# Kernel tuning notes

Hardware: AMD Instinct MI355X
Metric: run time of the kernel (lower is better)

The kernel has to match this reference:

```python
import jax, jax.numpy as jnp
import numpy as np

B, N, S, K, D = 8, 8192, 1024, 32, 64
RADIUS = 0.2
MLP = [64, 64, 128]
C_IN = 3 + D


def _fps(pts):
    # pts: [N,3] -> [S] farthest-point indices (deterministic start at index 0,
    # matching pytorch3d.sample_farthest_points default random_start_point=False)
    def body(carry, _):
        d, last = carry
        dd = jnp.sum((pts - pts[last]) ** 2, axis=-1)
        d = jnp.minimum(d, dd)
        return (d, jnp.argmax(d)), last
    init = (jnp.full((pts.shape[0],), 1e10, pts.dtype), jnp.asarray(0))
    _, idxs = jax.lax.scan(body, init, None, length=S)
    return idxs


def _ball_query(new_xyz, xyz):
    # new_xyz [B,S,3], xyz [B,N,3] -> idx [B,S,K]
    # classic PointNet++ ball query: first K points (by index order) within radius;
    # queries with fewer than K neighbors are padded by replicating the first hit.
    sqr = jnp.sum((new_xyz[:, :, None, :] - xyz[:, None, :, :]) ** 2, axis=-1)  # [B,S,N]
    cand = jnp.where(sqr <= RADIUS ** 2,
                     jnp.arange(N, dtype=jnp.int32)[None, None, :],
                     jnp.int32(N))
    idx = -jax.lax.top_k(-cand, K)[0]  # K smallest valid indices, ascending
    first = idx[..., :1]
    return jnp.where(idx == N, first, idx)


def _gather(arr, idx):
    # arr [B,N,C], idx [B,S,K] -> [B,S,K,C]
    return jax.vmap(lambda a, i: a[i])(arr, idx)


def _forward(xyz, points, attention, w0, b0, w1, b1, w2, b2):
    x = xyz.transpose(0, 2, 1)        # [B,N,3]
    p = points.transpose(0, 2, 1)     # [B,N,D]
    a = attention.transpose(0, 2, 1)  # [B,N,1]
    fps_idx = jax.vmap(_fps)(x)                      # [B,S]
    new_xyz = jax.vmap(lambda q, i: q[i])(x, fps_idx)  # [B,S,3]
    idx = _ball_query(new_xyz, x)                    # [B,S,K]
    g_norm = _gather(x, idx) - new_xyz[:, :, None, :]   # [B,S,K,3]
    feat = jnp.concatenate([g_norm, _gather(p, idx)], axis=-1)  # [B,S,K,3+D]
    new_att = jnp.mean(_gather(a, idx), axis=-2).reshape(x.shape[0], 1, -1)  # [B,1,S]
    # shared MLP (1x1 Conv2d == per-point dense), no BN (bn=False)
    h = jax.nn.relu(jnp.einsum('bskc,oc->bsko', feat, w0) + b0)
    h = jax.nn.relu(jnp.einsum('bskc,oc->bsko', h, w1) + b1)
    h = jax.nn.relu(jnp.einsum('bskc,oc->bsko', h, w2) + b2)
    new_points = jnp.max(h, axis=2)  # max-pool over nsample -> [B,S,C_out]
    return new_xyz.transpose(0, 2, 1), new_points.transpose(0, 2, 1), new_att


def setup_inputs() -> dict:
    key = jax.random.key(0)
    ks = jax.random.split(key, 9)
    xyz = jax.random.uniform(ks[0], (B, 3, N), dtype=jnp.float32)  # unit cube
    points = jax.random.normal(ks[1], (B, D, N), dtype=jnp.float32)
    attention = jax.random.uniform(ks[2], (B, 1, N), dtype=jnp.float32)
    cin = C_IN
    w0 = jax.random.normal(ks[3], (MLP[0], cin), dtype=jnp.float32) / np.sqrt(cin)
    b0 = jnp.zeros((MLP[0],), jnp.float32)
    w1 = jax.random.normal(ks[4], (MLP[1], MLP[0]), dtype=jnp.float32) / np.sqrt(MLP[0])
    b1 = jnp.zeros((MLP[1],), jnp.float32)
    w2 = jax.random.normal(ks[5], (MLP[2], MLP[1]), dtype=jnp.float32) / np.sqrt(MLP[1])
    b2 = jnp.zeros((MLP[2],), jnp.float32)
    return {"xyz": xyz, "points": points, "attention": attention,
            "w0": w0, "b0": b0, "w1": w1, "b1": b1, "w2": w2, "b2": b2}


def reference(xyz, points, attention, w0, b0, w1, b1, w2, b2):
    return _forward(xyz, points, attention, w0, b0, w1, b1, w2, b2)
```

## Files before the change

kernel.cpp:

```cpp
#include <hip/hip_runtime.h>

#define NPTS 8192
#define NSAMP 1024
#define NBATCH 8
#define KNB 32

typedef float f32x2 __attribute__((ext_vector_type(2)));
typedef unsigned long long u64;

__device__ __forceinline__ f32x2 pk_add(f32x2 a, f32x2 b) {
  f32x2 d; asm("v_pk_add_f32 %0, %1, %2" : "=v"(d) : "v"(a), "v"(b)); return d;
}
__device__ __forceinline__ f32x2 pk_mul(f32x2 a, f32x2 b) {
  f32x2 d; asm("v_pk_mul_f32 %0, %1, %2" : "=v"(d) : "v"(a), "v"(b)); return d;
}

#define DPP_FMAX_ROUND(v, CTRL)                                                        \
  do {                                                                                 \
    int _b = __float_as_int(v);                                                        \
    int _p = __builtin_amdgcn_update_dpp(_b, _b, CTRL, 0xF, 0xF, false);               \
    (v) = fmaxf((v), __int_as_float(_p));                                              \
  } while (0)

#define DPP_FMIN_ROUND(v, CTRL)                                                        \
  do {                                                                                 \
    int _b = __float_as_int(v);                                                        \
    int _p = __builtin_amdgcn_update_dpp(_b, _b, CTRL, 0xF, 0xF, false);               \
    (v) = fminf((v), __int_as_float(_p));                                              \
  } while (0)

#define DPP_UMIN_ROUND(v, CTRL)                                                        \
  do {                                                                                 \
    unsigned _p = (unsigned)__builtin_amdgcn_update_dpp((int)(v), (int)(v), CTRL,      \
                                                        0xF, 0xF, false);              \
    if (_p < (v)) (v) = _p;                                                            \
  } while (0)

#define DPP_MIN_ROUND(k, CTRL)                                                         \
  do {                                                                                 \
    unsigned _lo = (unsigned)(k), _hi = (unsigned)((k) >> 32);                         \
    unsigned _plo = (unsigned)__builtin_amdgcn_update_dpp((int)_lo, (int)_lo, CTRL,    \
                                                          0xF, 0xF, false);            \
    unsigned _phi = (unsigned)__builtin_amdgcn_update_dpp((int)_hi, (int)_hi, CTRL,    \
                                                          0xF, 0xF, false);            \
    u64 _ok = (((u64)_phi) << 32) | _plo;                                              \
    if (_ok < (k)) (k) = _ok;                                                          \
  } while (0)

__device__ __forceinline__ float sqdist_rn(float px, float py, float pz,
                                           float qx, float qy, float qz) {
  float dx = px - qx, dy = py - qy, dz = pz - qz;
  return __fadd_rn(__fadd_rn(__fmul_rn(dx, dx), __fmul_rn(dy, dy)), __fmul_rn(dz, dz));
}

__global__ __launch_bounds__(512) void fps_kernel(const float* __restrict__ xyz,
                                                  float* __restrict__ out_newxyz) {
  __shared__ __align__(16) char smem_raw[NPTS * 3 * 4];
  u64* sbuf = reinterpret_cast<u64*>(smem_raw);
  float* cds = reinterpret_cast<float*>(smem_raw);
  __shared__ u64 wkeys[2][8];

  const int b = blockIdx.x;
  const int tid = threadIdx.x;
  const int lane = tid & 63;
  const int wv = tid >> 6;
  const float* xb = xyz + (size_t)b * 3 * NPTS;

  for (int j = 0; j < 16; j++) {
    int n = tid + j * 512;
    float x = xb[n];
    sbuf[n] = (((u64)__float_as_uint(x)) << 32) | (u64)n;
  }
  __syncthreads();

  for (unsigned k = 2; k <= (unsigned)NPTS; k <<= 1) {
    for (unsigned jm = k >> 1; jm > 0; jm >>= 1) {
      for (int p = 0; p < 16; p++) {
        unsigned i = (unsigned)tid + (unsigned)p * 512u;
        unsigned ixj = i ^ jm;
        if (ixj > i) {
          u64 a = sbuf[i], c = sbuf[ixj];
          bool up = ((i & k) == 0);
          if ((a > c) == up) { sbuf[i] = c; sbuf[ixj] = a; }
        }
      }
      __syncthreads();
    }
  }

  f32x2 X2[8], Y2[8], Z2[8], D2[8];
  unsigned idxp[8];
  float txmin = 1e30f, txmax = -1e30f;
#pragma unroll
  for (int j = 0; j < 8; j++) {
    u64 k0 = sbuf[tid * 16 + 2 * j];
    u64 k1 = sbuf[tid * 16 + 2 * j + 1];
    unsigned n0 = (unsigned)k0 & 8191u, n1 = (unsigned)k1 & 8191u;
    float x0 = __uint_as_float((unsigned)(k0 >> 32));
    float x1 = __uint_as_float((unsigned)(k1 >> 32));
    X2[j].x = x0; X2[j].y = x1;
    Y2[j].x = xb[NPTS + n0];     Y2[j].y = xb[NPTS + n1];
    Z2[j].x = xb[2 * NPTS + n0]; Z2[j].y = xb[2 * NPTS + n1];
    D2[j].x = 1e10f;             D2[j].y = 1e10f;
    idxp[j] = n0 | (n1 << 16);
    txmin = fminf(txmin, fminf(x0, x1));
    txmax = fmaxf(txmax, fmaxf(x0, x1));
  }
  DPP_FMIN_ROUND(txmin, 0x111); DPP_FMIN_ROUND(txmin, 0x112);
  DPP_FMIN_ROUND(txmin, 0x114); DPP_FMIN_ROUND(txmin, 0x118);
  DPP_FMIN_ROUND(txmin, 0x142); DPP_FMIN_ROUND(txmin, 0x143);
  DPP_FMAX_ROUND(txmax, 0x111); DPP_FMAX_ROUND(txmax, 0x112);
  DPP_FMAX_ROUND(txmax, 0x114); DPP_FMAX_ROUND(txmax, 0x118);
  DPP_FMAX_ROUND(txmax, 0x142); DPP_FMAX_ROUND(txmax, 0x143);
  const float xlo = __int_as_float(__builtin_amdgcn_readlane(__float_as_int(txmin), 63));
  const float xhi = __int_as_float(__builtin_amdgcn_readlane(__float_as_int(txmax), 63));
  __syncthreads();

#pragma unroll
  for (int j = 0; j < 8; j++) {
    unsigned n0 = idxp[j] & 0xFFFFu, n1 = idxp[j] >> 16;
    cds[n0 * 3 + 0] = X2[j].x; cds[n0 * 3 + 1] = Y2[j].x; cds[n0 * 3 + 2] = Z2[j].x;
    cds[n1 * 3 + 0] = X2[j].y; cds[n1 * 3 + 1] = Y2[j].y; cds[n1 * 3 + 2] = Z2[j].y;
  }
  __syncthreads();

  float sx = cds[0], sy = cds[1], sz = cds[2];
  unsigned c0i = 0, c1i = 0;
  float bv_cache = 1e10f;
  u64 key_cache = ~0ull;

  for (int t = 0; t < NSAMP; t++) {
    float gap = fmaxf(fmaxf(xlo - sx, sx - xhi), 0.0f);
    float lb = __fmul_rn(gap, gap);

    if (lb < bv_cache) {
      f32x2 nqx, nqy, nqz;
      nqx.x = -sx; nqx.y = -sx;
      nqy.x = -sy; nqy.y = -sy;
      nqz.x = -sz; nqz.y = -sz;
      float bvx = -1.0f, bvy = -1.0f;
#pragma unroll
      for (int j = 0; j < 8; j++) {
        f32x2 dx = pk_add(X2[j], nqx);
        f32x2 dy = pk_add(Y2[j], nqy);
        f32x2 dz = pk_add(Z2[j], nqz);
        f32x2 dd = pk_add(pk_add(pk_mul(dx, dx), pk_mul(dy, dy)), pk_mul(dz, dz));
        float m0 = fminf(D2[j].x, dd.x);
        float m1 = fminf(D2[j].y, dd.y);
        D2[j].x = m0;
        D2[j].y = m1;
        bvx = fmaxf(bvx, m0);
        bvy = fmaxf(bvy, m1);
      }
      float bv = fmaxf(bvx, bvy);

      DPP_FMAX_ROUND(bv, 0x111);
      DPP_FMAX_ROUND(bv, 0x112);
      DPP_FMAX_ROUND(bv, 0x114);
      DPP_FMAX_ROUND(bv, 0x118);
      DPP_FMAX_ROUND(bv, 0x142);
      DPP_FMAX_ROUND(bv, 0x143);
      float wval = __int_as_float(__builtin_amdgcn_readlane(__float_as_int(bv), 63));

      unsigned cand = 0xFFFFFFFFu;
#pragma unroll
      for (int j = 0; j < 8; j++) {
        unsigned n0 = idxp[j] & 0xFFFFu, n1 = idxp[j] >> 16;
        if (D2[j].x == wval && n0 < cand) cand = n0;
        if (D2[j].y == wval && n1 < cand) cand = n1;
      }
      DPP_UMIN_ROUND(cand, 0x111);
      DPP_UMIN_ROUND(cand, 0x112);
      DPP_UMIN_ROUND(cand, 0x114);
      DPP_UMIN_ROUND(cand, 0x118);
      DPP_UMIN_ROUND(cand, 0x142);
      DPP_UMIN_ROUND(cand, 0x143);

      key_cache = (((u64)(~__float_as_uint(wval))) << 32) | (u64)cand;
      bv_cache = wval;
    }

    const int par = t & 1;
    if (lane == 63) wkeys[par][wv] = key_cache;
    __syncthreads();
    u64 k8 = wkeys[par][lane & 7];
    DPP_MIN_ROUND(k8, 0xB1);
    DPP_MIN_ROUND(k8, 0x4E);
    DPP_MIN_ROUND(k8, 0x141);
    unsigned wid = (unsigned)__builtin_amdgcn_readfirstlane((int)(unsigned)k8);

    if (t + 1 == tid) c0i = wid;
    if (t + 1 == tid + 512) c1i = wid;

    sx = cds[wid * 3 + 0];
    sy = cds[wid * 3 + 1];
    sz = cds[wid * 3 + 2];
  }

  {
    float ax = cds[c0i * 3 + 0], ay = cds[c0i * 3 + 1], az = cds[c0i * 3 + 2];
    float bx = cds[c1i * 3 + 0], by = cds[c1i * 3 + 1], bz = cds[c1i * 3 + 2];
    out_newxyz[(b * 3 + 0) * NSAMP + tid] = ax;
    out_newxyz[(b * 3 + 1) * NSAMP + tid] = ay;
    out_newxyz[(b * 3 + 2) * NSAMP + tid] = az;
    out_newxyz[(b * 3 + 0) * NSAMP + 512 + tid] = bx;
    out_newxyz[(b * 3 + 1) * NSAMP + 512 + tid] = by;
    out_newxyz[(b * 3 + 2) * NSAMP + 512 + tid] = bz;
  }
}

__global__ __launch_bounds__(256) void ballq_kernel(const float* __restrict__ xyz,
                                                    const float* __restrict__ att,
                                                    const float* __restrict__ newxyz,
                                                    int* __restrict__ idx_out,
                                                    float* __restrict__ att_out) {
  __shared__ int rowbuf[4][KNB];
  const int wv = threadIdx.x >> 6;
  const int lane = threadIdx.x & 63;
  const int g = blockIdx.x * 4 + wv;
  const int b = g >> 10;
  const int s = g & 1023;
  const float* xb = xyz + (size_t)b * 3 * NPTS;

  float qx = newxyz[(b * 3 + 0) * NSAMP + s];
  float qy = newxyz[(b * 3 + 1) * NSAMP + s];
  float qz = newxyz[(b * 3 + 2) * NSAMP + s];

  int have = 0;
  int firstn = 0;
  for (int c = 0; c < NPTS / 64; c++) {
    int n = c * 64 + lane;
    float dd = sqdist_rn(xb[n], xb[NPTS + n], xb[2 * NPTS + n], qx, qy, qz);
    bool inb = (dd <= 0.04f);
    unsigned long long m = __ballot(inb);
    if (have == 0 && m != 0ull) firstn = c * 64 + __builtin_ctzll(m);
    int pre = __popcll(m & ((1ull << lane) - 1ull));
    if (inb && (have + pre) < KNB) rowbuf[wv][have + pre] = n;
    have += __popcll(m);
    if (have >= KNB) break;
  }
  if (have > KNB) have = KNB;
  if (lane < KNB && lane >= have) rowbuf[wv][lane] = firstn;

  float av = 0.0f;
  if (lane < KNB) {
    int myidx = rowbuf[wv][lane];
    idx_out[(size_t)g * KNB + lane] = myidx;
    av = att[(size_t)b * NPTS + myidx];
  }
#pragma unroll
  for (int m = 1; m < 64; m <<= 1) av += __shfl_xor(av, m, 64);
  if (lane == 0) att_out[g] = av * 0.03125f;
}

__global__ __launch_bounds__(256) void mlp_kernel(
    const float* __restrict__ xyz, const float* __restrict__ pts,
    const float* __restrict__ newxyz, const int* __restrict__ idx,
    const float* __restrict__ w0, const float* __restrict__ b0,
    const float* __restrict__ w1, const float* __restrict__ b1,
    const float* __restrict__ w2, const float* __restrict__ b2,
    float* __restrict__ out_np) {
  const int g = blockIdx.x;
  const int b = g >> 10;
  const int s = g & 1023;
  const int t = threadIdx.x;

  __shared__ __align__(16) float feat[67 * 32];
  __shared__ __align__(16) float h0s[64 * 36];
  __shared__ __align__(16) float h1s[64 * 36];
  __shared__ int sidx[KNB];

  if (t < KNB) sidx[t] = idx[(size_t)g * KNB + t];
  __syncthreads();

  {
    int k = t & 31, rg = t >> 5;
    int n = sidx[k];
    const float* pb = pts + (size_t)b * 64 * NPTS;
    for (int r = rg; r < 67; r += 8) {
      float v;
      if (r < 3)
        v = xyz[((size_t)b * 3 + r) * NPTS + n] - newxyz[(b * 3 + r) * NSAMP + s];
      else
        v = pb[(size_t)(r - 3) * NPTS + n];
      feat[r * 32 + k] = v;
    }
  }
  __syncthreads();

  const int kq = t & 7;
  const int og = t >> 3;

  {
    float a0[8];
    float bu = b0[2 * og], bw = b0[2 * og + 1];
    a0[0] = a0[1] = a0[2] = a0[3] = bu;
    a0[4] = a0[5] = a0[6] = a0[7] = bw;
    const float* wr0 = w0 + (2 * og) * 67;
    const float* wr1 = wr0 + 67;
    for (int c = 0; c < 67; c++) {
      float4 f = *(const float4*)&feat[c * 32 + kq * 4];
      float u = wr0[c], v = wr1[c];
      a0[0] = fmaf(u, f.x, a0[0]); a0[1] = fmaf(u, f.y, a0[1]);
      a0[2] = fmaf(u, f.z, a0[2]); a0[3] = fmaf(u, f.w, a0[3]);
      a0[4] = fmaf(v, f.x, a0[4]); a0[5] = fmaf(v, f.y, a0[5]);
      a0[6] = fmaf(v, f.z, a0[6]); a0[7] = fmaf(v, f.w, a0[7]);
    }
    float4 r0, r1;
    r0.x = fmaxf(a0[0], 0.f); r0.y = fmaxf(a0[1], 0.f);
    r0.z = fmaxf(a0[2], 0.f); r0.w = fmaxf(a0[3], 0.f);
    r1.x = fmaxf(a0[4], 0.f); r1.y = fmaxf(a0[5], 0.f);
    r1.z = fmaxf(a0[6], 0.f); r1.w = fmaxf(a0[7], 0.f);
    *(float4*)&h0s[(2 * og) * 36 + kq * 4] = r0;
    *(float4*)&h0s[(2 * og + 1) * 36 + kq * 4] = r1;
  }
  __syncthreads();

  {
    float a1[8];
    float bu = b1[2 * og], bw = b1[2 * og + 1];
    a1[0] = a1[1] = a1[2] = a1[3] = bu;
    a1[4] = a1[5] = a1[6] = a1[7] = bw;
    const float* wr0 = w1 + (2 * og) * 64;
    const float* wr1 = wr0 + 64;
    for (int c = 0; c < 64; c++) {
      float4 f = *(const float4*)&h0s[c * 36 + kq * 4];
      float u = wr0[c], v = wr1[c];
      a1[0] = fmaf(u, f.x, a1[0]); a1[1] = fmaf(u, f.y, a1[1]);
      a1[2] = fmaf(u, f.z, a1[2]); a1[3] = fmaf(u, f.w, a1[3]);
      a1[4] = fmaf(v, f.x, a1[4]); a1[5] = fmaf(v, f.y, a1[5]);
      a1[6] = fmaf(v, f.z, a1[6]); a1[7] = fmaf(v, f.w, a1[7]);
    }
    float4 r0, r1;
    r0.x = fmaxf(a1[0], 0.f); r0.y = fmaxf(a1[1], 0.f);
    r0.z = fmaxf(a1[2], 0.f); r0.w = fmaxf(a1[3], 0.f);
    r1.x = fmaxf(a1[4], 0.f); r1.y = fmaxf(a1[5], 0.f);
    r1.z = fmaxf(a1[6], 0.f); r1.w = fmaxf(a1[7], 0.f);
    *(float4*)&h1s[(2 * og) * 36 + kq * 4] = r0;
    *(float4*)&h1s[(2 * og + 1) * 36 + kq * 4] = r1;
  }
  __syncthreads();

  {
    const int kq2 = t & 3;
    const int og2 = t >> 2;
    float a2[16];
    float bu = b2[2 * og2], bw = b2[2 * og2 + 1];
#pragma unroll
    for (int i = 0; i < 8; i++) { a2[i] = bu; a2[8 + i] = bw; }
    const float* wr0 = w2 + (2 * og2) * 64;
    const float* wr1 = wr0 + 64;
    for (int c = 0; c < 64; c++) {
      float4 fA = *(const float4*)&h1s[c * 36 + kq2 * 8];
      float4 fB = *(const float4*)&h1s[c * 36 + kq2 * 8 + 4];
      float u = wr0[c], v = wr1[c];
      a2[0] = fmaf(u, fA.x, a2[0]);  a2[1] = fmaf(u, fA.y, a2[1]);
      a2[2] = fmaf(u, fA.z, a2[2]);  a2[3] = fmaf(u, fA.w, a2[3]);
      a2[4] = fmaf(u, fB.x, a2[4]);  a2[5] = fmaf(u, fB.y, a2[5]);
      a2[6] = fmaf(u, fB.z, a2[6]);  a2[7] = fmaf(u, fB.w, a2[7]);
      a2[8] = fmaf(v, fA.x, a2[8]);  a2[9] = fmaf(v, fA.y, a2[9]);
      a2[10] = fmaf(v, fA.z, a2[10]); a2[11] = fmaf(v, fA.w, a2[11]);
      a2[12] = fmaf(v, fB.x, a2[12]); a2[13] = fmaf(v, fB.y, a2[13]);
      a2[14] = fmaf(v, fB.z, a2[14]); a2[15] = fmaf(v, fB.w, a2[15]);
    }
    float m0 = a2[0], m1 = a2[8];
#pragma unroll
    for (int i = 1; i < 8; i++) { m0 = fmaxf(m0, a2[i]); m1 = fmaxf(m1, a2[8 + i]); }
    m0 = fmaxf(m0, 0.f);
    m1 = fmaxf(m1, 0.f);
    m0 = fmaxf(m0, __shfl_xor(m0, 1, 64));
    m0 = fmaxf(m0, __shfl_xor(m0, 2, 64));
    m1 = fmaxf(m1, __shfl_xor(m1, 1, 64));
    m1 = fmaxf(m1, __shfl_xor(m1, 2, 64));
    if (kq2 == 0) {
      out_np[((size_t)b * 128 + 2 * og2) * NSAMP + s] = m0;
      out_np[((size_t)b * 128 + 2 * og2 + 1) * NSAMP + s] = m1;
    }
  }
}

extern "C" void kernel_launch(void* const* d_in, const int* in_sizes, int n_in,
                              void* d_out, int out_size, void* d_ws, size_t ws_size,
                              hipStream_t stream) {
  (void)in_sizes; (void)n_in; (void)out_size; (void)ws_size;
  const float* xyz = (const float*)d_in[0];
  const float* pts = (const float*)d_in[1];
  const float* att = (const float*)d_in[2];
  const float* w0 = (const float*)d_in[3];
  const float* b0 = (const float*)d_in[4];
  const float* w1 = (const float*)d_in[5];
  const float* b1 = (const float*)d_in[6];
  const float* w2 = (const float*)d_in[7];
  const float* b2 = (const float*)d_in[8];

  float* out = (float*)d_out;
  float* out_newxyz = out;
  float* out_newpts = out + NBATCH * 3 * NSAMP;
  float* out_att = out + NBATCH * 3 * NSAMP + NBATCH * 128 * NSAMP;
  int* idx_ws = (int*)d_ws;

  fps_kernel<<<NBATCH, 512, 0, stream>>>(xyz, out_newxyz);
  ballq_kernel<<<(NBATCH * NSAMP) / 4, 256, 0, stream>>>(xyz, att, out_newxyz, idx_ws, out_att);
  mlp_kernel<<<NBATCH * NSAMP, 256, 0, stream>>>(xyz, pts, out_newxyz, idx_ws,
                                                 w0, b0, w1, b1, w2, b2, out_newpts);
}
```

Measured before the change: 1.160 ms.

## Fuse ball query into MLP kernel and vectorize weight loads

Removes the separate ball-query kernel. Each MLP block's first wavefront now runs the ball query itself, writing neighbor indices straight to shared memory, which drops the idx workspace round trip and one launch. Weight rows in layers 1 and 2 are now read as float4 instead of scalar loads. The change also swaps the order of the candidate checks in the FPS tie-break loop, which has no speed effect. The cost is that the other three waves in each 256-thread block sit idle during the ball-query scan.

```diff
diff --git a/kernel.cpp b/kernel.cpp
--- a/kernel.cpp
+++ b/kernel.cpp
@@ -166,8 +166,8 @@
 #pragma unroll
       for (int j = 0; j < 8; j++) {
         unsigned n0 = idxp[j] & 0xFFFFu, n1 = idxp[j] >> 16;
+        if (D2[j].y == wval && n1 < cand) cand = n1;
         if (D2[j].x == wval && n0 < cand) cand = n0;
-        if (D2[j].y == wval && n1 < cand) cand = n1;
       }
       DPP_UMIN_ROUND(cand, 0x111);
       DPP_UMIN_ROUND(cand, 0x112);
@@ -209,57 +209,13 @@
   }
 }
 
-__global__ __launch_bounds__(256) void ballq_kernel(const float* __restrict__ xyz,
-                                                    const float* __restrict__ att,
-                                                    const float* __restrict__ newxyz,
-                                                    int* __restrict__ idx_out,
-                                                    float* __restrict__ att_out) {
-  __shared__ int rowbuf[4][KNB];
-  const int wv = threadIdx.x >> 6;
-  const int lane = threadIdx.x & 63;
-  const int g = blockIdx.x * 4 + wv;
-  const int b = g >> 10;
-  const int s = g & 1023;
-  const float* xb = xyz + (size_t)b * 3 * NPTS;
-
-  float qx = newxyz[(b * 3 + 0) * NSAMP + s];
-  float qy = newxyz[(b * 3 + 1) * NSAMP + s];
-  float qz = newxyz[(b * 3 + 2) * NSAMP + s];
-
-  int have = 0;
-  int firstn = 0;
-  for (int c = 0; c < NPTS / 64; c++) {
-    int n = c * 64 + lane;
-    float dd = sqdist_rn(xb[n], xb[NPTS + n], xb[2 * NPTS + n], qx, qy, qz);
-    bool inb = (dd <= 0.04f);
-    unsigned long long m = __ballot(inb);
-    if (have == 0 && m != 0ull) firstn = c * 64 + __builtin_ctzll(m);
-    int pre = __popcll(m & ((1ull << lane) - 1ull));
-    if (inb && (have + pre) < KNB) rowbuf[wv][have + pre] = n;
-    have += __popcll(m);
-    if (have >= KNB) break;
-  }
-  if (have > KNB) have = KNB;
-  if (lane < KNB && lane >= have) rowbuf[wv][lane] = firstn;
-
-  float av = 0.0f;
-  if (lane < KNB) {
-    int myidx = rowbuf[wv][lane];
-    idx_out[(size_t)g * KNB + lane] = myidx;
-    av = att[(size_t)b * NPTS + myidx];
-  }
-#pragma unroll
-  for (int m = 1; m < 64; m <<= 1) av += __shfl_xor(av, m, 64);
-  if (lane == 0) att_out[g] = av * 0.03125f;
-}
-
-__global__ __launch_bounds__(256) void mlp_kernel(
+__global__ __launch_bounds__(256) void sample_kernel(
     const float* __restrict__ xyz, const float* __restrict__ pts,
-    const float* __restrict__ newxyz, const int* __restrict__ idx,
+    const float* __restrict__ att, const float* __restrict__ newxyz,
     const float* __restrict__ w0, const float* __restrict__ b0,
     const float* __restrict__ w1, const float* __restrict__ b1,
     const float* __restrict__ w2, const float* __restrict__ b2,
-    float* __restrict__ out_np) {
+    float* __restrict__ out_np, float* __restrict__ att_out) {
   const int g = blockIdx.x;
   const int b = g >> 10;
   const int s = g & 1023;
@@ -269,8 +225,39 @@
   __shared__ __align__(16) float h0s[64 * 36];
   __shared__ __align__(16) float h1s[64 * 36];
   __shared__ int sidx[KNB];
-
-  if (t < KNB) sidx[t] = idx[(size_t)g * KNB + t];
+  __shared__ float qs[3];
+
+  const float* xb = xyz + (size_t)b * 3 * NPTS;
+
+  if (t < 64) {
+    const int lane = t;
+    float qx = newxyz[(b * 3 + 0) * NSAMP + s];
+    float qy = newxyz[(b * 3 + 1) * NSAMP + s];
+    float qz = newxyz[(b * 3 + 2) * NSAMP + s];
+    if (lane == 0) { qs[0] = qx; qs[1] = qy; qs[2] = qz; }
+
+    int have = 0;
+    int firstn = 0;
+    for (int c = 0; c < NPTS / 64; c++) {
+      int n = c * 64 + lane;
+      float dd = sqdist_rn(xb[n], xb[NPTS + n], xb[2 * NPTS + n], qx, qy, qz);
+      bool inb = (dd <= 0.04f);
+      unsigned long long m = __ballot(inb);
+      if (have == 0 && m != 0ull) firstn = c * 64 + __builtin_ctzll(m);
+      int pre = __popcll(m & ((1ull << lane) - 1ull));
+      if (inb && (have + pre) < KNB) sidx[have + pre] = n;
+      have += __popcll(m);
+      if (have >= KNB) break;
+    }
+    if (have > KNB) have = KNB;
+    if (lane < KNB && lane >= have) sidx[lane] = firstn;
+
+    float av = 0.0f;
+    if (lane < KNB) av = att[(size_t)b * NPTS + sidx[lane]];
+#pragma unroll
+    for (int m = 1; m < 64; m <<= 1) av += __shfl_xor(av, m, 64);
+    if (lane == 0) att_out[g] = av * 0.03125f;
+  }
   __syncthreads();
 
   {
@@ -280,7 +267,7 @@
     for (int r = rg; r < 67; r += 8) {
       float v;
       if (r < 3)
-        v = xyz[((size_t)b * 3 + r) * NPTS + n] - newxyz[(b * 3 + r) * NSAMP + s];
+        v = xyz[((size_t)b * 3 + r) * NPTS + n] - qs[r];
       else
         v = pb[(size_t)(r - 3) * NPTS + n];
       feat[r * 32 + k] = v;
@@ -321,15 +308,21 @@
     float bu = b1[2 * og], bw = b1[2 * og + 1];
     a1[0] = a1[1] = a1[2] = a1[3] = bu;
     a1[4] = a1[5] = a1[6] = a1[7] = bw;
-    const float* wr0 = w1 + (2 * og) * 64;
-    const float* wr1 = wr0 + 64;
-    for (int c = 0; c < 64; c++) {
-      float4 f = *(const float4*)&h0s[c * 36 + kq * 4];
-      float u = wr0[c], v = wr1[c];
-      a1[0] = fmaf(u, f.x, a1[0]); a1[1] = fmaf(u, f.y, a1[1]);
-      a1[2] = fmaf(u, f.z, a1[2]); a1[3] = fmaf(u, f.w, a1[3]);
-      a1[4] = fmaf(v, f.x, a1[4]); a1[5] = fmaf(v, f.y, a1[5]);
-      a1[6] = fmaf(v, f.z, a1[6]); a1[7] = fmaf(v, f.w, a1[7]);
+    const float4* wv0 = (const float4*)(w1 + (2 * og) * 64);
+    const float4* wv1 = (const float4*)(w1 + (2 * og + 1) * 64);
+    for (int c4 = 0; c4 < 16; c4++) {
+      float4 u4 = wv0[c4], v4 = wv1[c4];
+#pragma unroll
+      for (int i = 0; i < 4; i++) {
+        int c = c4 * 4 + i;
+        float u = (i == 0) ? u4.x : (i == 1) ? u4.y : (i == 2) ? u4.z : u4.w;
+        float v = (i == 0) ? v4.x : (i == 1) ? v4.y : (i == 2) ? v4.z : v4.w;
+        float4 f = *(const float4*)&h0s[c * 36 + kq * 4];
+        a1[0] = fmaf(u, f.x, a1[0]); a1[1] = fmaf(u, f.y, a1[1]);
+        a1[2] = fmaf(u, f.z, a1[2]); a1[3] = fmaf(u, f.w, a1[3]);
+        a1[4] = fmaf(v, f.x, a1[4]); a1[5] = fmaf(v, f.y, a1[5]);
+        a1[6] = fmaf(v, f.z, a1[6]); a1[7] = fmaf(v, f.w, a1[7]);
+      }
     }
     float4 r0, r1;
     r0.x = fmaxf(a1[0], 0.f); r0.y = fmaxf(a1[1], 0.f);
@@ -348,20 +341,26 @@
     float bu = b2[2 * og2], bw = b2[2 * og2 + 1];
 #pragma unroll
     for (int i = 0; i < 8; i++) { a2[i] = bu; a2[8 + i] = bw; }
-    const float* wr0 = w2 + (2 * og2) * 64;
-    const float* wr1 = wr0 + 64;
-    for (int c = 0; c < 64; c++) {
-      float4 fA = *(const float4*)&h1s[c * 36 + kq2 * 8];
-      float4 fB = *(const float4*)&h1s[c * 36 + kq2 * 8 + 4];
-      float u = wr0[c], v = wr1[c];
-      a2[0] = fmaf(u, fA.x, a2[0]);  a2[1] = fmaf(u, fA.y, a2[1]);
-      a2[2] = fmaf(u, fA.z, a2[2]);  a2[3] = fmaf(u, fA.w, a2[3]);
-      a2[4] = fmaf(u, fB.x, a2[4]);  a2[5] = fmaf(u, fB.y, a2[5]);
-      a2[6] = fmaf(u, fB.z, a2[6]);  a2[7] = fmaf(u, fB.w, a2[7]);
-      a2[8] = fmaf(v, fA.x, a2[8]);  a2[9] = fmaf(v, fA.y, a2[9]);
-      a2[10] = fmaf(v, fA.z, a2[10]); a2[11] = fmaf(v, fA.w, a2[11]);
-      a2[12] = fmaf(v, fB.x, a2[12]); a2[13] = fmaf(v, fB.y, a2[13]);
-      a2[14] = fmaf(v, fB.z, a2[14]); a2[15] = fmaf(v, fB.w, a2[15]);
+    const float4* wv0 = (const float4*)(w2 + (2 * og2) * 64);
+    const float4* wv1 = (const float4*)(w2 + (2 * og2 + 1) * 64);
+    for (int c4 = 0; c4 < 16; c4++) {
+      float4 u4 = wv0[c4], v4 = wv1[c4];
+#pragma unroll
+      for (int i = 0; i < 4; i++) {
+        int c = c4 * 4 + i;
+        float u = (i == 0) ? u4.x : (i == 1) ? u4.y : (i == 2) ? u4.z : u4.w;
+        float v = (i == 0) ? v4.x : (i == 1) ? v4.y : (i == 2) ? v4.z : v4.w;
+        float4 fA = *(const float4*)&h1s[c * 36 + kq2 * 8];
+        float4 fB = *(const float4*)&h1s[c * 36 + kq2 * 8 + 4];
+        a2[0] = fmaf(u, fA.x, a2[0]);  a2[1] = fmaf(u, fA.y, a2[1]);
+        a2[2] = fmaf(u, fA.z, a2[2]);  a2[3] = fmaf(u, fA.w, a2[3]);
+        a2[4] = fmaf(u, fB.x, a2[4]);  a2[5] = fmaf(u, fB.y, a2[5]);
+        a2[6] = fmaf(u, fB.z, a2[6]);  a2[7] = fmaf(u, fB.w, a2[7]);
+        a2[8] = fmaf(v, fA.x, a2[8]);  a2[9] = fmaf(v, fA.y, a2[9]);
+        a2[10] = fmaf(v, fA.z, a2[10]); a2[11] = fmaf(v, fA.w, a2[11]);
+        a2[12] = fmaf(v, fB.x, a2[12]); a2[13] = fmaf(v, fB.y, a2[13]);
+        a2[14] = fmaf(v, fB.z, a2[14]); a2[15] = fmaf(v, fB.w, a2[15]);
+      }
     }
     float m0 = a2[0], m1 = a2[8];
 #pragma unroll
@@ -382,7 +381,7 @@
 extern "C" void kernel_launch(void* const* d_in, const int* in_sizes, int n_in,
                               void* d_out, int out_size, void* d_ws, size_t ws_size,
                               hipStream_t stream) {
-  (void)in_sizes; (void)n_in; (void)out_size; (void)ws_size;
+  (void)in_sizes; (void)n_in; (void)out_size; (void)d_ws; (void)ws_size;
   const float* xyz = (const float*)d_in[0];
   const float* pts = (const float*)d_in[1];
   const float* att = (const float*)d_in[2];
@@ -397,10 +396,8 @@
   float* out_newxyz = out;
   float* out_newpts = out + NBATCH * 3 * NSAMP;
   float* out_att = out + NBATCH * 3 * NSAMP + NBATCH * 128 * NSAMP;
-  int* idx_ws = (int*)d_ws;
 
   fps_kernel<<<NBATCH, 512, 0, stream>>>(xyz, out_newxyz);
-  ballq_kernel<<<(NBATCH * NSAMP) / 4, 256, 0, stream>>>(xyz, att, out_newxyz, idx_ws, out_att);
-  mlp_kernel<<<NBATCH * NSAMP, 256, 0, stream>>>(xyz, pts, out_newxyz, idx_ws,
-                                                 w0, b0, w1, b1, w2, b2, out_newpts);
-}
+  sample_kernel<<<NBATCH * NSAMP, 256, 0, stream>>>(
+      xyz, pts, att, out_newxyz, w0, b0, w1, b1, w2, b2, out_newpts, out_att);
+}
```

After: 1.133 ms (median of 2 runs). 2.3% less time.
